# Kernel tuning notes

Hardware: AMD Instinct MI355X
Metric: run time of the kernel (lower is better)

Reference implementation:

```python
import jax, jax.numpy as jnp
import numpy as np
import math

D_MODEL = 1024
NUM_HEADS = 16
HEAD_DIM = D_MODEL // NUM_HEADS  # 64
THETA = 10000.0
BATCH = 2
SEQ = 2048


def setup_inputs() -> dict:
    key = jax.random.key(0)
    ks = jax.random.split(key, 5)
    scale = 0.02
    return {
        "in_features": jax.random.normal(ks[0], (BATCH, SEQ, D_MODEL), jnp.float32),
        "q_proj": jax.random.normal(ks[1], (D_MODEL, D_MODEL), jnp.float32) * scale,
        "k_proj": jax.random.normal(ks[2], (D_MODEL, D_MODEL), jnp.float32) * scale,
        "v_proj": jax.random.normal(ks[3], (D_MODEL, D_MODEL), jnp.float32) * scale,
        "o_proj": jax.random.normal(ks[4], (D_MODEL, D_MODEL), jnp.float32) * scale,
        "token_positions": jnp.arange(SEQ, dtype=jnp.int32),
    }


def _rope(x, token_positions):
    # x: [b, h, s, head_dim]; interleaved even/odd rotation
    half = HEAD_DIM // 2
    inv_freq = 1.0 / (THETA ** (2.0 * jnp.arange(half, dtype=x.dtype) / HEAD_DIM))
    angle = token_positions.astype(x.dtype)[:, None] * inv_freq[None, :]  # [s, half]
    cos, sin = jnp.cos(angle), jnp.sin(angle)
    x_e, x_o = x[..., ::2], x[..., 1::2]
    r_e = x_e * cos - x_o * sin
    r_o = x_e * sin + x_o * cos
    # interleave back: [..., s, half, 2] -> [..., s, head_dim]
    return jnp.stack([r_e, r_o], axis=-1).reshape(x.shape)


def reference(in_features, q_proj, k_proj, v_proj, o_proj, token_positions):
    b, s, _ = in_features.shape
    # projections: weight layout is [d_out, d_in]
    Q = jnp.einsum('bsd,kd->bsk', in_features, q_proj)
    K = jnp.einsum('bsd,kd->bsk', in_features, k_proj)
    V = jnp.einsum('bsd,kd->bsk', in_features, v_proj)
    # split heads: [b, h, s, head_dim]
    Q = Q.reshape(b, s, NUM_HEADS, HEAD_DIM).transpose(0, 2, 1, 3)
    K = K.reshape(b, s, NUM_HEADS, HEAD_DIM).transpose(0, 2, 1, 3)
    V = V.reshape(b, s, NUM_HEADS, HEAD_DIM).transpose(0, 2, 1, 3)
    Q = _rope(Q, token_positions)
    K = _rope(K, token_positions)
    scores = jnp.einsum('bhnd,bhmd->bhnm', Q, K) / math.sqrt(HEAD_DIM)
    causal = jnp.tril(jnp.ones((s, s), dtype=bool))  # [s, s]
    scores = jnp.where(causal[None, None], scores, -jnp.inf)
    attn = jax.nn.softmax(scores, axis=-1)
    out = jnp.einsum('bhnm,bhmd->bhnd', attn, V)
    out = out.transpose(0, 2, 1, 3).reshape(b, s, D_MODEL)
    return jnp.einsum('bsv,dv->bsd', out, o_proj)
```

## Files before the change

### kernel.cpp

```cpp
#include <hip/hip_runtime.h>
#include <hip/hip_bf16.h>
#include <hip/hip_cooperative_groups.h>

#define D_MODEL 1024
#define NHEAD   16
#define HDIM    64
#define SEQQ    2048
#define NBATCH  2
#define MROWS   (NBATCH * SEQQ)

typedef unsigned short u16;
typedef __attribute__((ext_vector_type(8))) short short8;
typedef __attribute__((ext_vector_type(4))) short bf16x4;
typedef __attribute__((ext_vector_type(4))) float floatx4;

__device__ __forceinline__ u16 f2b(float f) {
    union { __hip_bfloat16 h; u16 u; } cv;
    cv.h = __float2bfloat16(f);
    return cv.u;
}
__device__ __forceinline__ float b2f(u16 u) {
    return __uint_as_float(((unsigned int)u) << 16);
}
__device__ __forceinline__ short8 load8(const u16* p) {
    return *reinterpret_cast<const short8*>(p);
}
__device__ __forceinline__ bf16x4 load4v(const u16* p) {
    return *reinterpret_cast<const bf16x4*>(p);
}
__device__ __forceinline__ unsigned pack2(float lo, float hi) {
    return ((unsigned)f2b(hi) << 16) | (unsigned)f2b(lo);
}
__device__ __forceinline__ void async_cp16(const void* g, void* l) {
    __builtin_amdgcn_global_load_lds(
        (const __attribute__((address_space(1))) void*)g,
        (__attribute__((address_space(3))) void*)l, 16, 0, 0);
}


__device__ __forceinline__ void cvt_body(
    int bx, int zz, int tid,
    const float* X, const float* Wq, const float* Wk, const float* Wv,
    const float* Wo, const int* pos,
    u16* Xb, u16* WqB, u16* WkB, u16* WvB, u16* WoB, float2* tab)
{
    const int i = bx * 256 + tid;
    if (zz == 8) {
        if (i < SEQQ * 32) {
            const int j = i >> 11, s = i & (SEQQ - 1);
            const float p = (float)pos[s];
            const float inv = expf(-(float)j * (9.210340371976184f / 32.0f));
            float sn, cs;
            sincosf(p * inv, &sn, &cs);
            tab[i] = make_float2(cs, sn);
        }
        return;
    }
    const int n4 = (D_MODEL * D_MODEL) / 4;
    const float* in;
    u16* outp;
    if (zz < 4) { in = X + (size_t)zz * n4 * 4;  outp = Xb + (size_t)zz * n4 * 4; }
    else {
        in   = (zz == 4) ? Wq : (zz == 5) ? Wk : (zz == 6) ? Wv : Wo;
        outp = (zz == 4) ? WqB : (zz == 5) ? WkB : (zz == 6) ? WvB : WoB;
    }
    int src = i;
    if (zz == 4 || zz == 5) {
        const int orow = i >> 8;
        const int g    = i & 255;
        const int irow = (orow & ~63) | (((orow & 31) << 1) | ((orow >> 5) & 1));
        src = irow * 256 + g;
    }
    float4 v = reinterpret_cast<const float4*>(in)[src];
    ushort4 o;
    o.x = f2b(v.x); o.y = f2b(v.y); o.z = f2b(v.z); o.w = f2b(v.w);
    reinterpret_cast<ushort4*>(outp)[i] = o;
}

__device__ __forceinline__ void qkv_body(
    int bid, int tid, u16* smem,
    const u16* A, const u16* B0, const u16* B1, const u16* B2,
    u16* Qt, u16* Kt, u16* Vt, const float2* tab)
{
    const int K = D_MODEL;
    const int z  = bid >> 8;
    const int bx = bid & 31;
    const int by = (bid >> 5) & 7;
    const u16* Bt = (z == 0) ? B0 : (z == 1 ? B1 : B2);

    const int w    = tid >> 6;
    const int lane = tid & 63;
    const int l15  = lane & 15;
    const int quad = lane >> 4;
    const int wm   = w >> 1, wn = w & 1;
    const int tm   = bx * 128, tn = by * 128;

    floatx4 acc[4][4];
#pragma unroll
    for (int i = 0; i < 4; i++)
#pragma unroll
        for (int j = 0; j < 4; j++) {
            floatx4 zz4 = {0.f, 0.f, 0.f, 0.f};
            acc[i][j] = zz4;
        }

    const int srow = lane >> 2;
    const int scol = (lane & 3) * 8;

    auto stage = [&](int buf, int k0) {
#pragma unroll
        for (int ch = w; ch < 8; ch += 4) {
            async_cp16(A  + (size_t)(tm + ch * 16 + srow) * K + k0 + scol,
                       smem + buf * 4096 + ch * 512);
            async_cp16(Bt + (size_t)(tn + ch * 16 + srow) * K + k0 + scol,
                       smem + 8192 + buf * 4096 + ch * 512);
        }
    };

    stage(0, 0);

    for (int kt = 0; kt < 32; ++kt) {
        asm volatile("s_waitcnt vmcnt(0)" ::: "memory");
        __builtin_amdgcn_s_barrier();
        if (kt < 31) stage((kt + 1) & 1, (kt + 1) * 32);

        const u16* AsB = smem + (kt & 1) * 4096;
        const u16* BsB = smem + 8192 + (kt & 1) * 4096;

        short8 af[4], bfr[4];
#pragma unroll
        for (int mi = 0; mi < 4; mi++)
            af[mi] = load8(&AsB[(wm * 64 + mi * 16 + l15) * 32 + quad * 8]);
#pragma unroll
        for (int ni = 0; ni < 4; ni++)
            bfr[ni] = load8(&BsB[(wn * 64 + ni * 16 + l15) * 32 + quad * 8]);
#pragma unroll
        for (int mi = 0; mi < 4; mi++)
#pragma unroll
            for (int ni = 0; ni < 4; ni++)
                acc[mi][ni] = __builtin_amdgcn_mfma_f32_16x16x32_bf16(af[mi], bfr[ni], acc[mi][ni], 0, 0, 0);
    }

    if (z == 2) {
#pragma unroll
        for (int mi = 0; mi < 4; mi++) {
            const int r0 = tm + wm * 64 + mi * 16 + quad * 4;
            const int bb = r0 >> 11, s0 = r0 & (SEQQ - 1);
#pragma unroll
            for (int ni = 0; ni < 4; ni++) {
                const int colb = tn + wn * 64 + ni * 16 + l15;
                const int d = colb & 63, hh = colb >> 6;
                ushort4 pk;
                pk.x = f2b(acc[mi][ni][0]);
                pk.y = f2b(acc[mi][ni][1]);
                pk.z = f2b(acc[mi][ni][2]);
                pk.w = f2b(acc[mi][ni][3]);
                *reinterpret_cast<ushort4*>(
                    &Vt[(((size_t)(bb * NHEAD + hh)) * HDIM + d) * SEQQ + s0]) = pk;
            }
        }
    } else {
        const float qsc = (z == 0) ? 0.18033688011112042f : 1.0f;
        u16* Outp = (z == 0) ? Qt : Kt;
        const int hh = (tn >> 6) + wn;
        float4 ta[2], tb[2];
        auto ldtab = [&](int g) {
            const int mi = g >> 1, ni = g & 1;
            const int qq = ni * 16 + l15;
            const int s0 = (tm + wm * 64 + mi * 16 + quad * 4) & (SEQQ - 1);
            ta[g & 1] = *reinterpret_cast<const float4*>(&tab[qq * SEQQ + s0]);
            tb[g & 1] = *reinterpret_cast<const float4*>(&tab[qq * SEQQ + s0 + 2]);
        };
        ldtab(0);
#pragma unroll
        for (int g = 0; g < 8; ++g) {
            if (g < 7) ldtab(g + 1);
            const int mi = g >> 1, ni = g & 1;
            const int qq = ni * 16 + l15;
            const int r0 = tm + wm * 64 + mi * 16 + quad * 4;
            const int bb = r0 >> 11, s0 = r0 & (SEQQ - 1);
            const float4 A4 = ta[g & 1], B4 = tb[g & 1];
            const float cs[4] = {A4.x, A4.z, B4.x, B4.z};
            const float sn[4] = {A4.y, A4.w, B4.y, B4.w};
#pragma unroll
            for (int rg = 0; rg < 4; rg++) {
                const float e = acc[mi][ni][rg];
                const float o = acc[mi][ni + 2][rg];
                const unsigned val =
                    (unsigned)f2b((e * cs[rg] - o * sn[rg]) * qsc) |
                    ((unsigned)f2b((e * sn[rg] + o * cs[rg]) * qsc) << 16);
                *reinterpret_cast<unsigned*>(
                    &Outp[(((size_t)(bb * NHEAD + hh)) * SEQQ + (s0 + rg)) * HDIM + 2 * qq]) = val;
            }
        }
    }
}

__device__ __forceinline__ void attn_body(
    int bid, int tid, u16* smem,
    const u16* Qt, const u16* Kt, const u16* Vt, u16* Out)
{
    const int xcd = bid & 7;
    const int u   = bid >> 3;
    const int col = xcd * 4 + (u & 3);
    const int m   = u >> 2;
    int qsub;
    if      (m < 8)  qsub = 31 - m;
    else if (m < 16) qsub = m - 8;
    else if (m < 24) qsub = 39 - m;
    else             qsub = m - 16;
    const int h = col & (NHEAD - 1), b = col >> 4;

    const int w = tid >> 6, lane = tid & 63;
    const int l15 = lane & 15, quad = lane >> 4;
    const size_t bh = (size_t)(b * NHEAD + h);
    const u16* Qh = Qt + bh * SEQQ * HDIM;
    const u16* Kh = Kt + bh * SEQQ * HDIM;
    const u16* Vh = Vt + bh * HDIM * SEQQ;

    short8 ones;
#pragma unroll
    for (int i = 0; i < 8; i++) ones[i] = (short)0x3F80;

    const int rr  = lane >> 3;
    const int swz = ((lane & 7) ^ rr) * 8;
    auto stage = [&](int buf, int tt) {
        const int k0s = tt * 64;
        async_cp16(Kh + (size_t)(k0s + w * 8 + rr) * HDIM + swz,       smem + buf * 4096 + w * 512);
        async_cp16(Kh + (size_t)(k0s + (w + 4) * 8 + rr) * HDIM + swz, smem + buf * 4096 + (w + 4) * 512);
        async_cp16(Vh + (size_t)(w * 8 + rr) * SEQQ + k0s + swz,       smem + 8192 + buf * 4096 + w * 512);
        async_cp16(Vh + (size_t)((w + 4) * 8 + rr) * SEQQ + k0s + swz, smem + 8192 + buf * 4096 + (w + 4) * 512);
    };

    const int s7  = l15 & 7;
    const int sw1 = ((quad)     ^ s7) * 8;
    const int sw2 = ((quad + 4) ^ s7) * 8;
    const int vo0 = (((quad >> 1)    ) ^ s7) * 8 + (quad & 1) * 4;
    const int vo1 = (((quad >> 1) + 2) ^ s7) * 8 + (quad & 1) * 4;
    const int vo2 = (((quad >> 1) + 4) ^ s7) * 8 + (quad & 1) * 4;
    const int vo3 = (((quad >> 1) + 6) ^ s7) * 8 + (quad & 1) * 4;

    const int q0w   = qsub * 64 + w * 16;
    const int tmaxp = qsub;

    short8 qf[2];
#pragma unroll
    for (int kk = 0; kk < 2; kk++)
        qf[kk] = load8(&Qh[(size_t)(q0w + l15) * HDIM + kk * 32 + quad * 8]);

    floatx4 O[4];
    floatx4 l_acc = {0.f, 0.f, 0.f, 0.f};
#pragma unroll
    for (int c = 0; c < 4; c++) { floatx4 zz4 = {0.f, 0.f, 0.f, 0.f}; O[c] = zz4; }

    stage(0, 0);

    for (int t = 0; t <= tmaxp; ++t) {
        asm volatile("s_waitcnt vmcnt(0)" ::: "memory");
        __builtin_amdgcn_s_barrier();
        if (t < tmaxp) stage((t + 1) & 1, t + 1);

        const u16* KsB = smem + (t & 1) * 4096;
        const u16* VsB = smem + 8192 + (t & 1) * 4096;
        const int k0 = t * 64;

        floatx4 S[4];
        __builtin_amdgcn_s_setprio(1);
#pragma unroll
        for (int c = 0; c < 4; c++) {
            const int rowb = (c * 16 + l15) * 64;
            floatx4 zz4 = {0.f, 0.f, 0.f, 0.f};
            S[c] = __builtin_amdgcn_mfma_f32_16x16x32_bf16(load8(&KsB[rowb + sw1]), qf[0], zz4, 0, 0, 0);
            S[c] = __builtin_amdgcn_mfma_f32_16x16x32_bf16(load8(&KsB[rowb + sw2]), qf[1], S[c], 0, 0, 0);
        }
        __builtin_amdgcn_s_setprio(0);

        if (t == tmaxp) {
            const int q = q0w + l15;
#pragma unroll
            for (int c = 0; c < 4; c++)
#pragma unroll
                for (int r = 0; r < 4; r++)
                    if (k0 + c * 16 + quad * 4 + r > q) S[c][r] = -1e30f;
        }

#pragma unroll
        for (int c = 0; c < 4; c++)
#pragma unroll
            for (int r = 0; r < 4; r++)
                S[c][r] = __builtin_amdgcn_exp2f(S[c][r]);

        union { short8 v; unsigned u2[4]; } pf0, pf1;
        pf0.u2[0] = pack2(S[0][0], S[0][1]);
        pf0.u2[1] = pack2(S[0][2], S[0][3]);
        pf0.u2[2] = pack2(S[1][0], S[1][1]);
        pf0.u2[3] = pack2(S[1][2], S[1][3]);
        pf1.u2[0] = pack2(S[2][0], S[2][1]);
        pf1.u2[1] = pack2(S[2][2], S[2][3]);
        pf1.u2[2] = pack2(S[3][0], S[3][1]);
        pf1.u2[3] = pack2(S[3][2], S[3][3]);

        __builtin_amdgcn_s_setprio(1);
        l_acc = __builtin_amdgcn_mfma_f32_16x16x32_bf16(pf0.v, ones, l_acc, 0, 0, 0);
        l_acc = __builtin_amdgcn_mfma_f32_16x16x32_bf16(pf1.v, ones, l_acc, 0, 0, 0);

#pragma unroll
        for (int c2 = 0; c2 < 4; c2++) {
            const int rowb = (c2 * 16 + l15) * 64;
            bf16x4 a0 = load4v(&VsB[rowb + vo0]);
            bf16x4 a1 = load4v(&VsB[rowb + vo1]);
            bf16x4 a2 = load4v(&VsB[rowb + vo2]);
            bf16x4 a3 = load4v(&VsB[rowb + vo3]);
            short8 v0 = __builtin_shufflevector(a0, a1, 0, 1, 2, 3, 4, 5, 6, 7);
            short8 v1 = __builtin_shufflevector(a2, a3, 0, 1, 2, 3, 4, 5, 6, 7);
            O[c2] = __builtin_amdgcn_mfma_f32_16x16x32_bf16(pf0.v, v0, O[c2], 0, 0, 0);
            O[c2] = __builtin_amdgcn_mfma_f32_16x16x32_bf16(pf1.v, v1, O[c2], 0, 0, 0);
        }
        __builtin_amdgcn_s_setprio(0);
    }

    float inv_l[4];
#pragma unroll
    for (int r = 0; r < 4; r++) inv_l[r] = 1.0f / l_acc[r];

#pragma unroll
    for (int c2 = 0; c2 < 4; c2++)
#pragma unroll
        for (int r = 0; r < 4; r++) {
            const int q    = q0w + quad * 4 + r;
            const int colo = h * HDIM + c2 * 16 + l15;
            Out[(size_t)(b * SEQQ + q) * D_MODEL + colo] = f2b(O[c2][r] * inv_l[r]);
        }
}

__device__ __forceinline__ void gemmo_body(
    int bid, int tid, u16* smem,
    const u16* A, const u16* Bt, float* C)
{
    const int K = D_MODEL, N = D_MODEL;
    const int bx = bid & 63, by = bid >> 6;
    const int w    = tid >> 6;
    const int lane = tid & 63;
    const int l15  = lane & 15;
    const int quad = lane >> 4;
    const int wm   = w >> 1, wn = w & 1;
    const int tm   = bx * 64, tn = by * 64;

    floatx4 acc[2][2];
#pragma unroll
    for (int i = 0; i < 2; i++)
#pragma unroll
        for (int j = 0; j < 2; j++) {
            floatx4 z4 = {0.f, 0.f, 0.f, 0.f};
            acc[i][j] = z4;
        }

    const int srow = lane >> 2;
    const int scol = (lane & 3) * 8;

    auto stage = [&](int buf, int k0) {
        async_cp16(A  + (size_t)(tm + w * 16 + srow) * K + k0 + scol, smem + buf * 2048 + w * 512);
        async_cp16(Bt + (size_t)(tn + w * 16 + srow) * K + k0 + scol, smem + 6144 + buf * 2048 + w * 512);
    };

    stage(0, 0);
    stage(1, 32);

    for (int kt = 0; kt < 32; ++kt) {
        if (kt < 30) asm volatile("s_waitcnt vmcnt(2)" ::: "memory");
        else         asm volatile("s_waitcnt vmcnt(0)" ::: "memory");
        __builtin_amdgcn_s_barrier();
        if (kt < 30) stage((kt + 2) % 3, (kt + 2) * 32);

        const u16* AsB = smem + (kt % 3) * 2048;
        const u16* BsB = smem + 6144 + (kt % 3) * 2048;

        short8 af[2], bfr[2];
#pragma unroll
        for (int mi = 0; mi < 2; mi++)
            af[mi] = load8(&AsB[(wm * 32 + mi * 16 + l15) * 32 + quad * 8]);
#pragma unroll
        for (int ni = 0; ni < 2; ni++)
            bfr[ni] = load8(&BsB[(wn * 32 + ni * 16 + l15) * 32 + quad * 8]);
#pragma unroll
        for (int mi = 0; mi < 2; mi++)
#pragma unroll
            for (int ni = 0; ni < 2; ni++)
                acc[mi][ni] = __builtin_amdgcn_mfma_f32_16x16x32_bf16(af[mi], bfr[ni], acc[mi][ni], 0, 0, 0);
    }

#pragma unroll
    for (int mi = 0; mi < 2; mi++)
#pragma unroll
        for (int ni = 0; ni < 2; ni++)
#pragma unroll
            for (int rg = 0; rg < 4; rg++) {
                int row = tm + wm * 32 + mi * 16 + quad * 4 + rg;
                int colo = tn + wn * 32 + ni * 16 + l15;
                C[(size_t)row * N + colo] = acc[mi][ni][rg];
            }
}

__global__ __launch_bounds__(256, 4) void mega(
    const float* __restrict__ X,  const float* __restrict__ Wq,
    const float* __restrict__ Wk, const float* __restrict__ Wv,
    const float* __restrict__ Wo, const int* __restrict__ pos,
    u16* __restrict__ Xb,  u16* __restrict__ WqB, u16* __restrict__ WkB,
    u16* __restrict__ WvB, u16* __restrict__ WoB, float2* __restrict__ tab,
    u16* __restrict__ Qt, u16* __restrict__ Kt, u16* __restrict__ Vt,
    u16* __restrict__ AOut, float* __restrict__ out)
{
    cooperative_groups::grid_group grid = cooperative_groups::this_grid();
    __shared__ __attribute__((aligned(16))) u16 smem[16384];

    const int tid  = threadIdx.x;
    const int bid0 = blockIdx.x;

    for (int vb = bid0; vb < 9216; vb += 1024)
        cvt_body(vb & 1023, vb >> 10, tid, X, Wq, Wk, Wv, Wo, pos,
                 Xb, WqB, WkB, WvB, WoB, tab);
    __threadfence();
    grid.sync();

    if (bid0 < 768)
        qkv_body(bid0, tid, smem, Xb, WqB, WkB, WvB, Qt, Kt, Vt, tab);
    __threadfence();
    grid.sync();

    attn_body(bid0, tid, smem, Qt, Kt, Vt, AOut);
    __threadfence();
    grid.sync();

    gemmo_body(bid0, tid, smem, AOut, WoB, out);
}

__global__ void cvt_all_k(const float* __restrict__ X,
                          const float* __restrict__ w0, const float* __restrict__ w1,
                          const float* __restrict__ w2, const float* __restrict__ w3,
                          const int* __restrict__ pos,
                          u16* __restrict__ xo,
                          u16* __restrict__ o0, u16* __restrict__ o1,
                          u16* __restrict__ o2, u16* __restrict__ o3,
                          float2* __restrict__ tab) {
    cvt_body(blockIdx.x, blockIdx.y, threadIdx.x, X, w0, w1, w2, w3, pos,
             xo, o0, o1, o2, o3, tab);
}

__global__ __launch_bounds__(256) void gemm_qkv_k(
    const u16* __restrict__ A,
    const u16* __restrict__ B0, const u16* __restrict__ B1, const u16* __restrict__ B2,
    u16* __restrict__ Qt, u16* __restrict__ Kt, u16* __restrict__ Vt,
    const float2* __restrict__ tab)
{
    __shared__ __attribute__((aligned(16))) u16 smem[16384];
    const int bid = blockIdx.x + blockIdx.y * 32 + blockIdx.z * 256;
    qkv_body(bid, threadIdx.x, smem, A, B0, B1, B2, Qt, Kt, Vt, tab);
}

__global__ __launch_bounds__(256, 4) void attn_k(
    const u16* __restrict__ Qt, const u16* __restrict__ Kt, const u16* __restrict__ Vt,
    u16* __restrict__ Out)
{
    __shared__ __attribute__((aligned(16))) u16 smem[16384];
    attn_body(blockIdx.x, threadIdx.x, smem, Qt, Kt, Vt, Out);
}

__global__ __launch_bounds__(256) void gemm_o_k(
    const u16* __restrict__ A, const u16* __restrict__ Bt, float* __restrict__ C)
{
    __shared__ __attribute__((aligned(16))) u16 smem[12288];
    gemmo_body(blockIdx.x + blockIdx.y * 64, threadIdx.x, smem, A, Bt, C);
}

extern "C" void kernel_launch(void* const* d_in, const int* in_sizes, int n_in,
                              void* d_out, int out_size, void* d_ws, size_t ws_size,
                              hipStream_t stream)
{
    const float* X  = (const float*)d_in[0];
    const float* Wq = (const float*)d_in[1];
    const float* Wk = (const float*)d_in[2];
    const float* Wv = (const float*)d_in[3];
    const float* Wo = (const float*)d_in[4];
    const int* tpos = (const int*)d_in[5];
    float* out = (float*)d_out;
    char* ws = (char*)d_ws;

    const size_t MB = (size_t)1 << 20;
    u16*    Xb  = (u16*)(ws + 0);
    u16*    WqB = (u16*)(ws + 8 * MB);
    u16*    WkB = (u16*)(ws + 10 * MB);
    u16*    WvB = (u16*)(ws + 12 * MB);
    u16*    WoB = (u16*)(ws + 14 * MB);
    float2* tab = (float2*)(ws + 16 * MB);
    u16*    Qt  = (u16*)(ws + 24 * MB);
    u16*    Kt  = (u16*)(ws + 32 * MB);
    u16*    Vt  = (u16*)(ws + 40 * MB);
    u16*   AOut = (u16*)(ws + 48 * MB);

    static int use_coop = -1;
    if (use_coop < 0) {
        int nb = 0;
        hipError_t e = hipOccupancyMaxActiveBlocksPerMultiprocessor(
            &nb, reinterpret_cast<const void*>(&mega), 256, 0);
        int dev = 0, coop = 0;
        hipGetDevice(&dev);
        hipDeviceGetAttribute(&coop, hipDeviceAttributeCooperativeLaunch, dev);
        use_coop = (e == hipSuccess && nb >= 4 && coop) ? 1 : 0;
    }

    if (use_coop) {
        void* args[] = {
            (void*)&X, (void*)&Wq, (void*)&Wk, (void*)&Wv, (void*)&Wo, (void*)&tpos,
            (void*)&Xb, (void*)&WqB, (void*)&WkB, (void*)&WvB, (void*)&WoB, (void*)&tab,
            (void*)&Qt, (void*)&Kt, (void*)&Vt, (void*)&AOut, (void*)&out
        };
        hipLaunchCooperativeKernel(reinterpret_cast<const void*>(&mega),
                                   dim3(1024), dim3(256), args, 0, stream);
    } else {
        cvt_all_k<<<dim3(1024, 9), 256, 0, stream>>>(X, Wq, Wk, Wv, Wo, tpos,
                                                     Xb, WqB, WkB, WvB, WoB, tab);
        gemm_qkv_k<<<dim3(32, 8, 3), 256, 0, stream>>>(Xb, WqB, WkB, WvB,
                                                       Qt, Kt, Vt, tab);
        attn_k<<<dim3(1024, 1, 1), 256, 0, stream>>>(Qt, Kt, Vt, AOut);
        gemm_o_k<<<dim3(64, 16), 256, 0, stream>>>(AOut, WoB, out);
    }
}
```

Before: 174.4 us.

## Replace final grid barrier with per-row-block flags and dynamic O-proj tile queue

Removes the grid.sync between attention and the output projection. Each attention block bumps a per-(batch, query-block) counter in global memory. Blocks then take output-GEMM tiles from an atomic work queue and spin until the 16 heads feeding that row block are done. Causal attention is imbalanced, so this lets the O-projection start on finished rows while slower attention blocks are still running. The cost is atomic traffic, spin-waiting, and a reliance on the attention block-to-tile mapping being correct.

After: 174.4 us. No clear change (-0.0%).

```diff
diff --git a/kernel.cpp b/kernel.cpp
--- a/kernel.cpp
+++ b/kernel.cpp
@@ -408,10 +408,11 @@
     u16* __restrict__ Xb,  u16* __restrict__ WqB, u16* __restrict__ WkB,
     u16* __restrict__ WvB, u16* __restrict__ WoB, float2* __restrict__ tab,
     u16* __restrict__ Qt, u16* __restrict__ Kt, u16* __restrict__ Vt,
-    u16* __restrict__ AOut, float* __restrict__ out)
+    u16* __restrict__ AOut, float* __restrict__ out, int* __restrict__ flags)
 {
     cooperative_groups::grid_group grid = cooperative_groups::this_grid();
     __shared__ __attribute__((aligned(16))) u16 smem[16384];
+    __shared__ int s_tile;
 
     const int tid  = threadIdx.x;
     const int bid0 = blockIdx.x;
@@ -419,6 +420,7 @@
     for (int vb = bid0; vb < 9216; vb += 1024)
         cvt_body(vb & 1023, vb >> 10, tid, X, Wq, Wk, Wv, Wo, pos,
                  Xb, WqB, WkB, WvB, WoB, tab);
+    if (bid0 == 0 && tid < 65) flags[tid] = 0;
     __threadfence();
     grid.sync();
 
@@ -428,10 +430,39 @@
     grid.sync();
 
     attn_body(bid0, tid, smem, Qt, Kt, Vt, AOut);
-    __threadfence();
-    grid.sync();
-
-    gemmo_body(bid0, tid, smem, AOut, WoB, out);
+    {
+        const int xcd = bid0 & 7;
+        const int u   = bid0 >> 3;
+        const int col = xcd * 4 + (u & 3);
+        const int m   = u >> 2;
+        int qsub;
+        if      (m < 8)  qsub = 31 - m;
+        else if (m < 16) qsub = m - 8;
+        else if (m < 24) qsub = 39 - m;
+        else             qsub = m - 16;
+        const int bb = col >> 4;
+        __threadfence();
+        __syncthreads();
+        if (tid == 0) atomicAdd(&flags[bb * 32 + qsub], 1);
+    }
+
+    for (;;) {
+        __syncthreads();
+        if (tid == 0) s_tile = atomicAdd(&flags[64], 1);
+        __syncthreads();
+        const int i = s_tile;
+        if (i >= 1024) break;
+        const int gq = i >> 4, ny = i & 15;
+        const int qs = gq >> 1, bb2 = gq & 1;
+        const int bx = bb2 * 32 + qs;
+        if (tid == 0) {
+            while (atomicOr(&flags[bx], 0) < 16)
+                __builtin_amdgcn_s_sleep(8);
+        }
+        __syncthreads();
+        __threadfence();
+        gemmo_body(bx | (ny << 6), tid, smem, AOut, WoB, out);
+    }
 }
 
 __global__ void cvt_all_k(const float* __restrict__ X,
@@ -496,6 +527,7 @@
     u16*    Kt  = (u16*)(ws + 32 * MB);
     u16*    Vt  = (u16*)(ws + 40 * MB);
     u16*   AOut = (u16*)(ws + 48 * MB);
+    int*  flags = (int*)(ws + 56 * MB);
 
     static int use_coop = -1;
     if (use_coop < 0) {
@@ -512,7 +544,7 @@
         void* args[] = {
             (void*)&X, (void*)&Wq, (void*)&Wk, (void*)&Wv, (void*)&Wo, (void*)&tpos,
             (void*)&Xb, (void*)&WqB, (void*)&WkB, (void*)&WvB, (void*)&WoB, (void*)&tab,
-            (void*)&Qt, (void*)&Kt, (void*)&Vt, (void*)&AOut, (void*)&out
+            (void*)&Qt, (void*)&Kt, (void*)&Vt, (void*)&AOut, (void*)&out, (void*)&flags
         };
         hipLaunchCooperativeKernel(reinterpret_cast<const void*>(&mega),
                                    dim3(1024), dim3(256), args, 0, stream);
```
